# Performance work log

Hardware: AMD Instinct MI355X
Metric: run time of the kernel (lower is better)

Reference implementation:

```python
import jax, jax.numpy as jnp
import numpy as np

N_NODES = 200_000          # clusters (len(matched))
N_EDGES = 12_800_000       # bipartite assigned->others edges, avg degree 64
THRESH = 0.5               # assign_clusters default used by forward()


def setup_inputs() -> dict:
    key = jax.random.key(0)
    k1, k2, k3 = jax.random.split(key, 3)
    half = N_NODES // 2
    # bipartite incidence: sources are already-assigned primaries, dests are unassigned
    src = jax.random.randint(k1, (N_EDGES,), 0, half, dtype=jnp.int64)
    dst = jax.random.randint(k2, (N_EDGES,), half, N_NODES, dtype=jnp.int64)
    edge_index = jnp.stack([src, dst])                  # [2, E]
    edge_pred = jax.random.uniform(k3, (N_EDGES,), dtype=jnp.float32)  # [E]
    # matched: primaries point to themselves, everyone else is -1
    matched = jnp.concatenate([
        jnp.arange(half, dtype=jnp.int64),
        jnp.full((N_NODES - half,), -1, dtype=jnp.int64),
    ])
    return {"edge_pred": edge_pred, "edge_index": edge_index, "matched": matched}


def reference(edge_pred, edge_index, matched):
    """Vectorized IterativeEdgeModel.assign_clusters.

    For every unmatched node i (matched[i] == -1): among incoming edges
    (edge_index[1] == i) take the argmax of edge_pred (first max on ties, as
    torch.argmax); if that prediction > THRESH, set
    matched[i] = matched[edge_index[0, argmax_edge]].
    Returns (new_matched [N] int, win_pred [N] float, found_match scalar bool).
    """
    n = matched.shape[0]
    e = edge_pred.shape[0]
    src, dst = edge_index[0], edge_index[1]

    # per-destination max prediction (identity -inf where a node has no edges)
    best = jax.ops.segment_max(edge_pred, dst, num_segments=n)        # [N]
    # first edge index attaining the per-dst max (torch.argmax tie-break)
    cand = jnp.where(edge_pred == best[dst], jnp.arange(e), e)
    win_edge = jax.ops.segment_min(cand, dst, num_segments=n)         # [N], e if none
    has_edge = win_edge < e
    win_safe = jnp.where(has_edge, win_edge, 0)
    win_pred = jnp.where(has_edge, edge_pred[win_safe], jnp.float32(0))  # [N]

    is_other = matched == -1
    update = is_other & has_edge & (win_pred > THRESH)                # [N] bool
    # sources are in the assigned partition, so matched[src] is fixed this pass
    new_matched = jnp.where(update, matched[src[win_safe]], matched)
    found_match = jnp.any(update)
    return new_matched, win_pred, found_match
```

## Files before the change

### kernel.cpp

```cpp
#include <hip/hip_runtime.h>
#include <string.h>


typedef float fx4 __attribute__((ext_vector_type(4)));
typedef int   ix4 __attribute__((ext_vector_type(4)));

#define CH 4

__device__ __forceinline__ unsigned long long pack64(unsigned pbits, unsigned i) {
    return ((unsigned long long)pbits << 32) |
           (unsigned long long)(0xFFFFFFFFu - i);
}

__device__ __forceinline__ unsigned shadow_ld(const unsigned* p) {
    return __hip_atomic_load(p, __ATOMIC_RELAXED, __HIP_MEMORY_SCOPE_WORKGROUP);
}
__device__ __forceinline__ void shadow_st(unsigned* p, unsigned v) {
    __hip_atomic_store(p, v, __ATOMIC_RELAXED, __HIP_MEMORY_SCOPE_WORKGROUP);
}

__global__ void seed_pass(const float* __restrict__ pred,
                          const int* __restrict__ dst,
                          unsigned* __restrict__ shd,
                          int e, unsigned tseed) {
    const int nvec = e >> 2;
    const int T = gridDim.x * blockDim.x;
    const int t = blockIdx.x * blockDim.x + threadIdx.x;

    fx4 p[CH];
    ix4 d[CH];
    int vi[CH];
    bool ok[CH];
    #pragma unroll
    for (int c = 0; c < CH; ++c) {
        vi[c] = t + c * T;
        ok[c] = vi[c] < nvec;
        int a = ok[c] ? vi[c] : 0;
        p[c] = ((const fx4*)pred)[a];
        d[c] = ((const ix4*)dst)[a];
    }
    #pragma unroll
    for (int c = 0; c < CH; ++c) {
        unsigned pbv[4] = {__float_as_uint(p[c].x), __float_as_uint(p[c].y),
                           __float_as_uint(p[c].z), __float_as_uint(p[c].w)};
        int dv[4] = {d[c].x, d[c].y, d[c].z, d[c].w};
        #pragma unroll
        for (int k = 0; k < 4; ++k) {
            if (ok[c] && pbv[k] >= tseed)
                (void)__hip_atomic_fetch_max(&shd[dv[k]], pbv[k],
                                             __ATOMIC_RELAXED,
                                             __HIP_MEMORY_SCOPE_AGENT);
        }
    }
}

__global__ void bitmap_pass(const unsigned* __restrict__ shd,
                            unsigned long long* __restrict__ bmp,
                            int n, unsigned tseed) {
    int node = blockIdx.x * blockDim.x + threadIdx.x;
    bool set = (node < n) && (shd[node] >= tseed);
    unsigned long long mask = __ballot(set);
    if ((threadIdx.x & 63) == 0) {
        int w = node >> 6;
        if (w < ((n + 63) >> 6)) bmp[w] = mask;
    }
}

template <bool BMP>
__global__ void main_pass(const float* __restrict__ pred,
                          const int* __restrict__ dst,
                          unsigned long long* __restrict__ tbl,
                          unsigned* __restrict__ shd,
                          const unsigned long long* __restrict__ bmp,
                          int e, int n, unsigned tbits) {
    extern __shared__ unsigned long long lbmp[];
    const int nwords = (n + 63) >> 6;
    if (BMP) {
        for (int w = threadIdx.x; w < nwords; w += blockDim.x)
            lbmp[w] = bmp[w];
        __syncthreads();
    }

    const int nvec = e >> 2;
    const int T = gridDim.x * blockDim.x;
    const int t = blockIdx.x * blockDim.x + threadIdx.x;

    fx4 p[CH];
    ix4 d[CH];
    int vi[CH];
    bool ok[CH];
    #pragma unroll
    for (int c = 0; c < CH; ++c) {
        vi[c] = t + c * T;
        ok[c] = vi[c] < nvec;
        int a = ok[c] ? vi[c] : 0;
        p[c] = ((const fx4*)pred)[a];
        d[c] = ((const ix4*)dst)[a];
    }

    #pragma unroll
    for (int c = 0; c < CH; ++c) {
        unsigned pbv[4] = {__float_as_uint(p[c].x), __float_as_uint(p[c].y),
                           __float_as_uint(p[c].z), __float_as_uint(p[c].w)};
        int dv[4] = {d[c].x, d[c].y, d[c].z, d[c].w};
        unsigned base = (unsigned)(vi[c] << 2);

        bool slow[4];
        unsigned cc[4] = {0, 0, 0, 0};
        #pragma unroll
        for (int k = 0; k < 4; ++k) {
            bool seeded = false;
            if (BMP)
                seeded = (lbmp[dv[k] >> 6] >> (dv[k] & 63)) & 1ULL;
            slow[k] = ok[c] && !(seeded && pbv[k] < tbits);
        }
        #pragma unroll
        for (int k = 0; k < 4; ++k)
            if (slow[k]) cc[k] = shadow_ld(&shd[dv[k]]);
        #pragma unroll
        for (int k = 0; k < 4; ++k) {
            if (slow[k] && pbv[k] >= cc[k]) {
                (void)__hip_atomic_fetch_max(&tbl[dv[k]],
                                             pack64(pbv[k], base + k),
                                             __ATOMIC_RELAXED,
                                             __HIP_MEMORY_SCOPE_AGENT);
                shadow_st(&shd[dv[k]], pbv[k]);
            }
        }
    }

    if (blockIdx.x == 0 && threadIdx.x == 0) {
        for (int i = (nvec << 2); i < e; ++i) {
            unsigned pb_ = __float_as_uint(pred[i]);
            int dd = dst[i];
            if (pb_ >= shadow_ld(&shd[dd])) {
                (void)__hip_atomic_fetch_max(&tbl[dd], pack64(pb_, (unsigned)i),
                                             __ATOMIC_RELAXED,
                                             __HIP_MEMORY_SCOPE_AGENT);
                shadow_st(&shd[dd], pb_);
            }
        }
    }
}

__global__ void node_kernel(const unsigned long long* __restrict__ best,
                            const int* __restrict__ matched,
                            const int* __restrict__ src,
                            float* __restrict__ out_matched,
                            float* __restrict__ out_winpred,
                            float* __restrict__ found,
                            int n) {
    int i = blockIdx.x * blockDim.x + threadIdx.x;
    if (i >= n) return;
    unsigned long long b = best[i];
    int m = matched[i];
    int nm = m;
    float wp = 0.0f;
    if (b != 0ULL) {
        wp = __uint_as_float((unsigned int)(b >> 32));
        unsigned int idx = 0xFFFFFFFFu - (unsigned int)(b & 0xFFFFFFFFu);
        if (m == -1 && wp > 0.5f) {
            nm = matched[src[idx]];
            *found = 1.0f;
        }
    }
    out_matched[i] = (float)nm;
    out_winpred[i] = wp;
}

extern "C" void kernel_launch(void* const* d_in, const int* in_sizes, int n_in,
                              void* d_out, int out_size, void* d_ws, size_t ws_size,
                              hipStream_t stream) {
    const float* edge_pred = (const float*)d_in[0];
    const int*   edge_index = (const int*)d_in[1];
    const int*   matched   = (const int*)d_in[2];

    const int e = in_sizes[0];
    const int n = in_sizes[2];

    const int* src = edge_index;
    const int* dst = edge_index + e;

    unsigned long long* tbl = (unsigned long long*)d_ws;
    unsigned* shd = (unsigned*)(tbl + n);
    unsigned long long* bmp = (unsigned long long*)(shd + n);
    const int nwords = (n + 63) >> 6;

    float* out_matched = (float*)d_out;
    float* out_winpred = out_matched + n;
    float* found       = out_matched + 2 * n;

    (void)hipMemsetAsync(tbl, 0, (size_t)n * 12, stream);
    (void)hipMemsetAsync(found, 0, sizeof(float), stream);

    float ts = 0.97f;
    unsigned tseed;
    memcpy(&tseed, &ts, sizeof(tseed));

    const int block = 512;
    const int nvec = e >> 2;
    const int nthreads = (nvec + CH - 1) / CH;
    int grid_e = (nthreads + block - 1) / block;
    if (grid_e < 1) grid_e = 1;

    seed_pass<<<grid_e, block, 0, stream>>>(edge_pred, dst, shd, e, tseed);

    const size_t lds_bytes = (size_t)nwords * sizeof(unsigned long long);
    const bool use_bmp = lds_bytes <= 48 * 1024 &&
                         ws_size >= (size_t)n * 12 + lds_bytes;
    if (use_bmp) {
        int grid_b = (n + block - 1) / block;
        bitmap_pass<<<grid_b, block, 0, stream>>>(shd, bmp, n, tseed);
        main_pass<true><<<grid_e, block, lds_bytes, stream>>>(
            edge_pred, dst, tbl, shd, bmp, e, n, tseed);
    } else {
        main_pass<false><<<grid_e, block, 0, stream>>>(
            edge_pred, dst, tbl, shd, bmp, e, n, tseed);
    }

    int grid_n = (n + 255) / 256;
    node_kernel<<<grid_n, 256, 0, stream>>>(tbl, matched, src,
                                            out_matched, out_winpred, found, n);
}
```

Baseline: 71.32 us.

## Seed packed table directly in seed pass and gather dst only for high preds

The seed pass now writes the full packed (pred, index) entry into the result table for predictions above the threshold. It loads the destination index only for those sparse edges, so it no longer streams the whole dst array. The main pass then handles only sub-threshold edges at unseeded nodes, because the seed pass has already inserted the high edges, and the bitmap is derived from the table. The threshold moves from 0.97 to 0.98, and the non-bitmap fallback path is removed. That removal makes the code assume the bitmap always fits in LDS.

Result: no change. 70.95 us (-0.5%).

```diff
diff --git a/kernel.cpp b/kernel.cpp
--- a/kernel.cpp
+++ b/kernel.cpp
@@ -21,44 +21,43 @@
 
 __global__ void seed_pass(const float* __restrict__ pred,
                           const int* __restrict__ dst,
-                          unsigned* __restrict__ shd,
-                          int e, unsigned tseed) {
+                          unsigned long long* __restrict__ tbl,
+                          int e, unsigned tbits) {
     const int nvec = e >> 2;
     const int T = gridDim.x * blockDim.x;
     const int t = blockIdx.x * blockDim.x + threadIdx.x;
 
     fx4 p[CH];
-    ix4 d[CH];
     int vi[CH];
     bool ok[CH];
     #pragma unroll
     for (int c = 0; c < CH; ++c) {
         vi[c] = t + c * T;
         ok[c] = vi[c] < nvec;
-        int a = ok[c] ? vi[c] : 0;
-        p[c] = ((const fx4*)pred)[a];
-        d[c] = ((const ix4*)dst)[a];
+        p[c] = ((const fx4*)pred)[ok[c] ? vi[c] : 0];
     }
     #pragma unroll
     for (int c = 0; c < CH; ++c) {
         unsigned pbv[4] = {__float_as_uint(p[c].x), __float_as_uint(p[c].y),
                            __float_as_uint(p[c].z), __float_as_uint(p[c].w)};
-        int dv[4] = {d[c].x, d[c].y, d[c].z, d[c].w};
+        unsigned base = (unsigned)(vi[c] << 2);
         #pragma unroll
         for (int k = 0; k < 4; ++k) {
-            if (ok[c] && pbv[k] >= tseed)
-                (void)__hip_atomic_fetch_max(&shd[dv[k]], pbv[k],
+            if (ok[c] && pbv[k] >= tbits) {
+                int d = dst[base + k];
+                (void)__hip_atomic_fetch_max(&tbl[d], pack64(pbv[k], base + k),
                                              __ATOMIC_RELAXED,
                                              __HIP_MEMORY_SCOPE_AGENT);
-        }
-    }
-}
-
-__global__ void bitmap_pass(const unsigned* __restrict__ shd,
+            }
+        }
+    }
+}
+
+__global__ void bitmap_pass(const unsigned long long* __restrict__ tbl,
                             unsigned long long* __restrict__ bmp,
-                            int n, unsigned tseed) {
+                            int n, unsigned tbits) {
     int node = blockIdx.x * blockDim.x + threadIdx.x;
-    bool set = (node < n) && (shd[node] >= tseed);
+    bool set = (node < n) && ((unsigned)(tbl[node] >> 32) >= tbits);
     unsigned long long mask = __ballot(set);
     if ((threadIdx.x & 63) == 0) {
         int w = node >> 6;
@@ -66,7 +65,6 @@
     }
 }
 
-template <bool BMP>
 __global__ void main_pass(const float* __restrict__ pred,
                           const int* __restrict__ dst,
                           unsigned long long* __restrict__ tbl,
@@ -75,11 +73,9 @@
                           int e, int n, unsigned tbits) {
     extern __shared__ unsigned long long lbmp[];
     const int nwords = (n + 63) >> 6;
-    if (BMP) {
-        for (int w = threadIdx.x; w < nwords; w += blockDim.x)
-            lbmp[w] = bmp[w];
-        __syncthreads();
-    }
+    for (int w = threadIdx.x; w < nwords; w += blockDim.x)
+        lbmp[w] = bmp[w];
+    __syncthreads();
 
     const int nvec = e >> 2;
     const int T = gridDim.x * blockDim.x;
@@ -109,10 +105,9 @@
         unsigned cc[4] = {0, 0, 0, 0};
         #pragma unroll
         for (int k = 0; k < 4; ++k) {
-            bool seeded = false;
-            if (BMP)
-                seeded = (lbmp[dv[k] >> 6] >> (dv[k] & 63)) & 1ULL;
-            slow[k] = ok[c] && !(seeded && pbv[k] < tbits);
+            bool low = ok[c] && (pbv[k] < tbits);
+            bool seeded = (lbmp[dv[k] >> 6] >> (dv[k] & 63)) & 1ULL;
+            slow[k] = low && !seeded;
         }
         #pragma unroll
         for (int k = 0; k < 4; ++k)
@@ -193,9 +188,9 @@
     (void)hipMemsetAsync(tbl, 0, (size_t)n * 12, stream);
     (void)hipMemsetAsync(found, 0, sizeof(float), stream);
 
-    float ts = 0.97f;
-    unsigned tseed;
-    memcpy(&tseed, &ts, sizeof(tseed));
+    float ts = 0.98f;
+    unsigned tbits;
+    memcpy(&tbits, &ts, sizeof(tbits));
 
     const int block = 512;
     const int nvec = e >> 2;
@@ -203,20 +198,14 @@
     int grid_e = (nthreads + block - 1) / block;
     if (grid_e < 1) grid_e = 1;
 
-    seed_pass<<<grid_e, block, 0, stream>>>(edge_pred, dst, shd, e, tseed);
+    seed_pass<<<grid_e, block, 0, stream>>>(edge_pred, dst, tbl, e, tbits);
+
+    int grid_b = (n + block - 1) / block;
+    bitmap_pass<<<grid_b, block, 0, stream>>>(tbl, bmp, n, tbits);
 
     const size_t lds_bytes = (size_t)nwords * sizeof(unsigned long long);
-    const bool use_bmp = lds_bytes <= 48 * 1024 &&
-                         ws_size >= (size_t)n * 12 + lds_bytes;
-    if (use_bmp) {
-        int grid_b = (n + block - 1) / block;
-        bitmap_pass<<<grid_b, block, 0, stream>>>(shd, bmp, n, tseed);
-        main_pass<true><<<grid_e, block, lds_bytes, stream>>>(
-            edge_pred, dst, tbl, shd, bmp, e, n, tseed);
-    } else {
-        main_pass<false><<<grid_e, block, 0, stream>>>(
-            edge_pred, dst, tbl, shd, bmp, e, n, tseed);
-    }
+    main_pass<<<grid_e, block, lds_bytes, stream>>>(
+        edge_pred, dst, tbl, shd, bmp, e, n, tbits);
 
     int grid_n = (n + 255) / 256;
     node_kernel<<<grid_n, 256, 0, stream>>>(tbl, matched, src,
```
